# Kernel optimization log

Hardware: AMD Instinct MI355X
Metric: run time of the kernel (lower is better)

Reference implementation:

```python
import jax, jax.numpy as jnp
import numpy as np
from jax import lax

KS = 11          # kernel_size
SIGMA = 1.5
MAX_VAL = 1.0
C1 = (0.01 * MAX_VAL) ** 2
C2 = (0.03 * MAX_VAL) ** 2
EPS = 1e-12
PAD = KS // 2    # use_padding=True -> reflect pad


def _gaussian_kernel3d():
    ax = jnp.arange(KS, dtype=jnp.float32) - (KS - 1) / 2.0
    g = jnp.exp(-(ax[:, None, None] ** 2 + ax[None, :, None] ** 2 + ax[None, None, :] ** 2)
                / (2.0 * SIGMA ** 2))
    return g / g.sum()  # (KS, KS, KS)


def setup_inputs() -> dict:
    key = jax.random.key(0)
    k1, k2 = jax.random.split(key)
    shape = (2, 1, 160, 160, 160)
    source = jax.random.uniform(k1, shape, dtype=jnp.float32)
    reference_vol = jax.random.uniform(k2, shape, dtype=jnp.float32)
    return {"source": source, "reference": reference_vol}


def reference(source, reference):
    B, C, H, W, D = source.shape
    # reflect pad spatial dims (torch 'reflect' == numpy 'reflect')
    pad_cfg = ((0, 0), (0, 0), (PAD, PAD), (PAD, PAD), (PAD, PAD))
    src = jnp.pad(source, pad_cfg, mode="reflect")
    ref = jnp.pad(reference, pad_cfg, mode="reflect")

    # fuse the 5 depthwise convolutions into one grouped conv over stacked channels
    stacked = jnp.concatenate([src, ref, src * src, ref * ref, src * ref], axis=1)  # (B,5C,...)
    kern = _gaussian_kernel3d()[None, None]                      # (1,1,KS,KS,KS)
    kern = jnp.tile(kern, (5 * C, 1, 1, 1, 1))                   # (5C,1,KS,KS,KS)
    out = lax.conv_general_dilated(
        stacked, kern, window_strides=(1, 1, 1), padding="VALID",
        feature_group_count=5 * C,
        dimension_numbers=("NCDHW", "OIDHW", "NCDHW"))           # (B,5C,H,W,D)

    mu1 = out[:, 0 * C:1 * C]
    mu2 = out[:, 1 * C:2 * C]
    m11 = out[:, 2 * C:3 * C]
    m22 = out[:, 3 * C:4 * C]
    m12 = out[:, 4 * C:5 * C]

    mu1_sq = mu1 * mu1
    mu2_sq = mu2 * mu2
    mu1_mu2 = mu1 * mu2
    sigma1_sq = m11 - mu1_sq
    sigma2_sq = m22 - mu2_sq
    sigma12 = m12 - mu1_mu2

    numerator = (2.0 * mu1_mu2 + C1) * (2.0 * sigma12 + C2)
    denominator = (mu1_sq + mu2_sq + C1) * (sigma1_sq + sigma2_sq + C2)
    ssim = numerator / (denominator + EPS)
    return 1.0 - ssim.mean()
```

## Files before the change

kernel.cpp:

```cpp
#include <hip/hip_runtime.h>
#include <math.h>

#define HH 160
#define WW 160
#define DD 160
#define VOL (HH*WW*DD)
#define KS 11
#define PAD 5
#define NBATCH 2
#define NTOT (NBATCH*VOL)

#define WT 16
#define DT 16
#define HT 32
#define WPN (WT + 2*PAD)
#define NSTEP (HT + 2*PAD)
#define RS 68
#define P01S 36
#define P4S 16
#define RAW_W (WPN*RS)
#define P01_W (WPN*P01S)
#define P4_W  (WPN*P4S)

typedef float v2f __attribute__((ext_vector_type(2)));
typedef float v4f __attribute__((ext_vector_type(4)));

struct Wts { float w[KS]; };

__device__ __forceinline__ int mirror(int i, int n) {
    if (i < 0) i = -i;
    if (i >= n) i = 2*n - 2 - i;
    return i;
}

__device__ __forceinline__ v2f pk_fma(v2f a, v2f b, v2f c) {
    v2f d; asm("v_pk_fma_f32 %0, %1, %2, %3" : "=v"(d) : "v"(a), "v"(b), "v"(c)); return d;
}
__device__ __forceinline__ v2f pk_mul(v2f a, v2f b) {
    v2f d; asm("v_pk_mul_f32 %0, %1, %2" : "=v"(d) : "v"(a), "v"(b)); return d;
}
__device__ __forceinline__ v2f pk_add(v2f a, v2f b) {
    v2f d; asm("v_pk_add_f32 %0, %1, %2" : "=v"(d) : "v"(a), "v"(b)); return d;
}

__global__ void init_out(float* out) {
    if (threadIdx.x == 0 && blockIdx.x == 0) out[0] = 1.0f;
}

__global__ __launch_bounds__(256) void fused(const float* __restrict__ src,
                                             const float* __restrict__ ref,
                                             float* __restrict__ out,
                                             Wts wts, float scale) {
    __shared__ float raw [2*RAW_W];
    __shared__ float pl01[2*P01_W];
    __shared__ float pl23[2*P01_W];
    __shared__ float pl4 [2*P4_W];

    const int bx  = blockIdx.x;
    const int dt_ = bx % (DD/DT);
    const int wt_ = (bx / (DD/DT)) % (WW/WT);
    const int ht_ = (bx / ((DD/DT)*(WW/WT))) % (HH/HT);
    const int b   = bx / ((DD/DT)*(WW/WT)*(HH/HT));
    const int d0 = dt_*DT, w0 = wt_*WT, h0 = ht_*HT;

    const int  dbase = (d0 == 0) ? 0 : ((d0 == DD-DT) ? DD-32 : d0-8);
    const bool dedge = (d0 == 0) || (d0 == DD-DT);

    const int tid = threadIdx.x;
    const float* __restrict__ sp = src + (size_t)b*VOL;
    const float* __restrict__ rp = ref + (size_t)b*VOL;

    const bool sact = (tid < WPN*8);
    const int  swp = tid >> 3, sq = tid & 7;
    const int  sgoff  = mirror(w0 - PAD + (sact ? swp : 0), WW)*DD + dbase + sq*4;
    const int  srawof = swp*RS + sq*8;

    const int  p_dl  = tid & 15;
    const int  p_wp0 = tid >> 4;
    const bool p_act1 = (tid < WPN*DT - 256);
    const int  pw0_01 = p_wp0*P01S + 2*p_dl;
    const int  pw0_4  = p_wp0*P4S  + p_dl;
    const int  pw1_01 = (p_wp0+16)*P01S + 2*p_dl;
    const int  pw1_4  = (p_wp0+16)*P4S  + p_dl;

    int eoff[KS];
    if (dedge) {
#pragma unroll
        for (int k = 0; k < KS; ++k)
            eoff[k] = 2*(mirror(d0 + p_dl - PAD + k, DD) - dbase);
    }

    const int wl = tid >> 4, dl2 = tid & 15;

    v2f wpk[KS];
#pragma unroll
    for (int k = 0; k < KS; ++k) { wpk[k].x = wts.w[k]; wpk[k].y = wts.w[k]; }

    v2f acc01[KS], acc23[KS];
    float acc4[KS];
#pragma unroll
    for (int s = 0; s < KS; ++s) {
        acc01[s] = (v2f)0.f; acc23[s] = (v2f)0.f; acc4[s] = 0.f;
    }

    v4f ra = (v4f)0.f, rb_ = (v4f)0.f;
    if (sact) {
        const size_t o0 = (size_t)mirror(h0 - PAD, HH)*(WW*DD) + sgoff;
        ra  = *reinterpret_cast<const v4f*>(sp + o0);
        rb_ = *reinterpret_cast<const v4f*>(rp + o0);
        v4f c0, c1;
        c0.x=ra.x; c0.y=rb_.x; c0.z=ra.y; c0.w=rb_.y;
        c1.x=ra.z; c1.y=rb_.z; c1.z=ra.w; c1.w=rb_.w;
        *reinterpret_cast<v4f*>(&raw[srawof])     = c0;
        *reinterpret_cast<v4f*>(&raw[srawof + 4]) = c1;
        const size_t o1 = (size_t)mirror(h0 - PAD + 1, HH)*(WW*DD) + sgoff;
        ra  = *reinterpret_cast<const v4f*>(sp + o1);
        rb_ = *reinterpret_cast<const v4f*>(rp + o1);
    }
    __syncthreads();

    float ssum = 0.f;
    int rawRd = 0, rawWr = RAW_W, po01 = 0, po4 = 0;

    for (int tb = 0; tb < 44; tb += 11) {
#pragma unroll
        for (int ts = 0; ts < 11; ++ts) {
            const int t = tb + ts;
            if (t < NSTEP) {
                if (sact) {
                    v4f c0, c1;
                    c0.x=ra.x; c0.y=rb_.x; c0.z=ra.y; c0.w=rb_.y;
                    c1.x=ra.z; c1.y=rb_.z; c1.z=ra.w; c1.w=rb_.w;
                    *reinterpret_cast<v4f*>(&raw[rawWr + srawof])     = c0;
                    *reinterpret_cast<v4f*>(&raw[rawWr + srawof + 4]) = c1;
                    const size_t on = (size_t)mirror(h0 - PAD + t + 2, HH)*(WW*DD) + sgoff;
                    ra  = *reinterpret_cast<const v4f*>(sp + on);
                    rb_ = *reinterpret_cast<const v4f*>(rp + on);
                }

                v2f mu_a=(v2f)0.f, mm_a=(v2f)0.f, mu_b=(v2f)0.f, mm_b=(v2f)0.f;
                float m12a=0.f, m12b=0.f;
                if (!dedge) {
                    const float* r0 = &raw[rawRd + p_wp0*RS + 2*p_dl + 6];
                    const float* r1 = r0 + 16*RS;
#pragma unroll
                    for (int k = 0; k < KS; ++k) {
                        v2f sr = *reinterpret_cast<const v2f*>(r0 + 2*k);
                        v2f p  = pk_mul(sr, wpk[k]);
                        mu_a = pk_add(mu_a, p);
                        mm_a = pk_fma(p, sr, mm_a);
                        m12a = fmaf(p.x, sr.y, m12a);
                    }
                    if (p_act1) {
#pragma unroll
                        for (int k = 0; k < KS; ++k) {
                            v2f sr = *reinterpret_cast<const v2f*>(r1 + 2*k);
                            v2f p  = pk_mul(sr, wpk[k]);
                            mu_b = pk_add(mu_b, p);
                            mm_b = pk_fma(p, sr, mm_b);
                            m12b = fmaf(p.x, sr.y, m12b);
                        }
                    }
                } else {
                    const float* rb0 = &raw[rawRd + p_wp0*RS];
                    const float* rb1 = rb0 + 16*RS;
#pragma unroll
                    for (int k = 0; k < KS; ++k) {
                        v2f sr = *reinterpret_cast<const v2f*>(rb0 + eoff[k]);
                        v2f p  = pk_mul(sr, wpk[k]);
                        mu_a = pk_add(mu_a, p);
                        mm_a = pk_fma(p, sr, mm_a);
                        m12a = fmaf(p.x, sr.y, m12a);
                        if (p_act1) {
                            v2f sr2 = *reinterpret_cast<const v2f*>(rb1 + eoff[k]);
                            v2f p2  = pk_mul(sr2, wpk[k]);
                            mu_b = pk_add(mu_b, p2);
                            mm_b = pk_fma(p2, sr2, mm_b);
                            m12b = fmaf(p2.x, sr2.y, m12b);
                        }
                    }
                }
                *reinterpret_cast<v2f*>(&pl01[po01 + pw0_01]) = mu_a;
                *reinterpret_cast<v2f*>(&pl23[po01 + pw0_01]) = mm_a;
                pl4[po4 + pw0_4] = m12a;
                if (p_act1) {
                    *reinterpret_cast<v2f*>(&pl01[po01 + pw1_01]) = mu_b;
                    *reinterpret_cast<v2f*>(&pl23[po01 + pw1_01]) = mm_b;
                    pl4[po4 + pw1_4] = m12b;
                }

                __syncthreads();

                {
                    v2f v01 = (v2f)0.f, v23 = (v2f)0.f;
                    float v4v = 0.f;
                    const float* q01 = &pl01[po01 + wl*P01S + 2*dl2];
                    const float* q23 = &pl23[po01 + wl*P01S + 2*dl2];
                    const float* q4  = &pl4 [po4  + wl*P4S  + dl2];
#pragma unroll
                    for (int k = 0; k < KS; ++k) {
                        v2f w = wpk[k];
                        v01 = pk_fma(*reinterpret_cast<const v2f*>(q01 + k*P01S), w, v01);
                        v23 = pk_fma(*reinterpret_cast<const v2f*>(q23 + k*P01S), w, v23);
                        v4v = fmaf(w.x, q4[k*P4S], v4v);
                    }
#pragma unroll
                    for (int m = 0; m < 11; ++m) {
                        const int slot = (ts + m) % 11;
                        v2f wt = wpk[10 - m];
                        acc01[slot] = pk_fma(v01, wt, acc01[slot]);
                        acc23[slot] = pk_fma(v23, wt, acc23[slot]);
                        acc4[slot]  = fmaf(wt.x, v4v, acc4[slot]);
                    }
                    if (t >= 10) {
                        float mu1 = acc01[ts].x, mu2 = acc01[ts].y;
                        float m11 = acc23[ts].x, m22 = acc23[ts].y, m12 = acc4[ts];
                        float mu1sq = mu1*mu1, mu2sq = mu2*mu2, mu12 = mu1*mu2;
                        float s1 = m11 - mu1sq, s2 = m22 - mu2sq, s12 = m12 - mu12;
                        const float C1 = 1e-4f, C2 = 9e-4f;
                        float num = (2.f*mu12 + C1) * (2.f*s12 + C2);
                        float den = (mu1sq + mu2sq + C1) * (s1 + s2 + C2) + 1e-12f;
                        float inv = __builtin_amdgcn_rcpf(den);
                        inv = inv * (2.0f - den * inv);
                        ssum = fmaf(num, inv, ssum);
                    }
                    acc01[ts] = (v2f)0.f; acc23[ts] = (v2f)0.f; acc4[ts] = 0.f;
                }

                rawRd ^= RAW_W; rawWr ^= RAW_W; po01 ^= P01_W; po4 ^= P4_W;
            }
        }
    }

#pragma unroll
    for (int off = 32; off > 0; off >>= 1)
        ssum += __shfl_down(ssum, off, 64);
    __shared__ float lsum[4];
    int lane = tid & 63, wid = tid >> 6;
    if (lane == 0) lsum[wid] = ssum;
    __syncthreads();
    if (tid == 0)
        atomicAdd(out, -(lsum[0]+lsum[1]+lsum[2]+lsum[3]) * scale);
}

extern "C" void kernel_launch(void* const* d_in, const int* in_sizes, int n_in,
                              void* d_out, int out_size, void* d_ws, size_t ws_size,
                              hipStream_t stream) {
    const float* src = (const float*)d_in[0];
    const float* ref = (const float*)d_in[1];
    float* out = (float*)d_out;

    Wts wts;
    {
        double g[KS], s = 0.0;
        for (int i = 0; i < KS; ++i) {
            double a = (double)i - (KS - 1) / 2.0;
            g[i] = exp(-(a * a) / (2.0 * 1.5 * 1.5));
            s += g[i];
        }
        for (int i = 0; i < KS; ++i) wts.w[i] = (float)(g[i] / s);
    }

    const float scale = 1.0f / (float)NTOT;

    init_out<<<1, 64, 0, stream>>>(out);
    const int g = NBATCH * (HH/HT) * (WW/WT) * (DD/DT);
    fused<<<g, 256, 0, stream>>>(src, ref, out, wts, scale);
}
```

Before: 212.5 us.

## Compute two adjacent depth outputs per thread in first conv pass

The depth-direction convolution pass now gives each of the 208 active threads two adjacent depth outputs (8 threads per W row). Each thread reads 12 shared-memory values and reuses them for both outputs, where before a thread did one output and some threads made a second pass over a separate row. The change also switches the packed FMA/add inline asm to in-place accumulator constraints, adds a launch_bounds occupancy hint of 4 blocks, and aligns the shared arrays. The aim is fewer LDS reads and better thread balance, at the cost of more registers per thread and a possible bank-conflict shift from the wider stores.

```diff
diff --git a/kernel.cpp b/kernel.cpp
--- a/kernel.cpp
+++ b/kernel.cpp
@@ -33,28 +33,28 @@
     return i;
 }
 
-__device__ __forceinline__ v2f pk_fma(v2f a, v2f b, v2f c) {
-    v2f d; asm("v_pk_fma_f32 %0, %1, %2, %3" : "=v"(d) : "v"(a), "v"(b), "v"(c)); return d;
+__device__ __forceinline__ void pk_fma_acc(v2f& c, v2f a, v2f b) {
+    asm("v_pk_fma_f32 %0, %1, %2, %0" : "+v"(c) : "v"(a), "v"(b));
+}
+__device__ __forceinline__ void pk_add_acc(v2f& c, v2f a) {
+    asm("v_pk_add_f32 %0, %0, %1" : "+v"(c) : "v"(a));
 }
 __device__ __forceinline__ v2f pk_mul(v2f a, v2f b) {
     v2f d; asm("v_pk_mul_f32 %0, %1, %2" : "=v"(d) : "v"(a), "v"(b)); return d;
 }
-__device__ __forceinline__ v2f pk_add(v2f a, v2f b) {
-    v2f d; asm("v_pk_add_f32 %0, %1, %2" : "=v"(d) : "v"(a), "v"(b)); return d;
-}
 
 __global__ void init_out(float* out) {
     if (threadIdx.x == 0 && blockIdx.x == 0) out[0] = 1.0f;
 }
 
-__global__ __launch_bounds__(256) void fused(const float* __restrict__ src,
-                                             const float* __restrict__ ref,
-                                             float* __restrict__ out,
-                                             Wts wts, float scale) {
-    __shared__ float raw [2*RAW_W];
-    __shared__ float pl01[2*P01_W];
-    __shared__ float pl23[2*P01_W];
-    __shared__ float pl4 [2*P4_W];
+__global__ __launch_bounds__(256, 4) void fused(const float* __restrict__ src,
+                                                const float* __restrict__ ref,
+                                                float* __restrict__ out,
+                                                Wts wts, float scale) {
+    __shared__ __align__(16) float raw [2*RAW_W];
+    __shared__ __align__(16) float pl01[2*P01_W];
+    __shared__ __align__(16) float pl23[2*P01_W];
+    __shared__ __align__(16) float pl4 [2*P4_W];
 
     const int bx  = blockIdx.x;
     const int dt_ = bx % (DD/DT);
@@ -75,19 +75,17 @@
     const int  sgoff  = mirror(w0 - PAD + (sact ? swp : 0), WW)*DD + dbase + sq*4;
     const int  srawof = swp*RS + sq*8;
 
-    const int  p_dl  = tid & 15;
-    const int  p_wp0 = tid >> 4;
-    const bool p_act1 = (tid < WPN*DT - 256);
-    const int  pw0_01 = p_wp0*P01S + 2*p_dl;
-    const int  pw0_4  = p_wp0*P4S  + p_dl;
-    const int  pw1_01 = (p_wp0+16)*P01S + 2*p_dl;
-    const int  pw1_4  = (p_wp0+16)*P4S  + p_dl;
-
-    int eoff[KS];
+    const int  p_wp  = tid >> 3;
+    const int  p_dlp = tid & 7;
+    const int  pA01  = p_wp*P01S + 4*p_dlp;
+    const int  pA4   = p_wp*P4S  + 2*p_dlp;
+    const int  p_rbase = p_wp*RS + 6 + 4*p_dlp;
+
+    int eoff[12];
     if (dedge) {
 #pragma unroll
-        for (int k = 0; k < KS; ++k)
-            eoff[k] = 2*(mirror(d0 + p_dl - PAD + k, DD) - dbase);
+        for (int j = 0; j < 12; ++j)
+            eoff[j] = 2*(mirror(d0 + 2*p_dlp - PAD + j, DD) - dbase);
     }
 
     const int wl = tid >> 4, dl2 = tid & 15;
@@ -136,57 +134,52 @@
                     const size_t on = (size_t)mirror(h0 - PAD + t + 2, HH)*(WW*DD) + sgoff;
                     ra  = *reinterpret_cast<const v4f*>(sp + on);
                     rb_ = *reinterpret_cast<const v4f*>(rp + on);
-                }
-
-                v2f mu_a=(v2f)0.f, mm_a=(v2f)0.f, mu_b=(v2f)0.f, mm_b=(v2f)0.f;
-                float m12a=0.f, m12b=0.f;
-                if (!dedge) {
-                    const float* r0 = &raw[rawRd + p_wp0*RS + 2*p_dl + 6];
-                    const float* r1 = r0 + 16*RS;
-#pragma unroll
-                    for (int k = 0; k < KS; ++k) {
-                        v2f sr = *reinterpret_cast<const v2f*>(r0 + 2*k);
-                        v2f p  = pk_mul(sr, wpk[k]);
-                        mu_a = pk_add(mu_a, p);
-                        mm_a = pk_fma(p, sr, mm_a);
-                        m12a = fmaf(p.x, sr.y, m12a);
-                    }
-                    if (p_act1) {
-#pragma unroll
-                        for (int k = 0; k < KS; ++k) {
-                            v2f sr = *reinterpret_cast<const v2f*>(r1 + 2*k);
-                            v2f p  = pk_mul(sr, wpk[k]);
-                            mu_b = pk_add(mu_b, p);
-                            mm_b = pk_fma(p, sr, mm_b);
-                            m12b = fmaf(p.x, sr.y, m12b);
+
+                    v2f muA=(v2f)0.f, mmA=(v2f)0.f, muB=(v2f)0.f, mmB=(v2f)0.f;
+                    float m12A=0.f, m12B=0.f;
+                    if (!dedge) {
+                        const float* r0 = &raw[rawRd + p_rbase];
+#pragma unroll
+                        for (int j = 0; j < 12; ++j) {
+                            v2f sr = *reinterpret_cast<const v2f*>(r0 + 2*j);
+                            if (j < 11) {
+                                v2f p = pk_mul(sr, wpk[j]);
+                                pk_add_acc(muA, p);
+                                pk_fma_acc(mmA, p, sr);
+                                m12A = fmaf(p.x, sr.y, m12A);
+                            }
+                            if (j > 0) {
+                                v2f p = pk_mul(sr, wpk[j-1]);
+                                pk_add_acc(muB, p);
+                                pk_fma_acc(mmB, p, sr);
+                                m12B = fmaf(p.x, sr.y, m12B);
+                            }
                         }
-                    }
-                } else {
-                    const float* rb0 = &raw[rawRd + p_wp0*RS];
-                    const float* rb1 = rb0 + 16*RS;
-#pragma unroll
-                    for (int k = 0; k < KS; ++k) {
-                        v2f sr = *reinterpret_cast<const v2f*>(rb0 + eoff[k]);
-                        v2f p  = pk_mul(sr, wpk[k]);
-                        mu_a = pk_add(mu_a, p);
-                        mm_a = pk_fma(p, sr, mm_a);
-                        m12a = fmaf(p.x, sr.y, m12a);
-                        if (p_act1) {
-                            v2f sr2 = *reinterpret_cast<const v2f*>(rb1 + eoff[k]);
-                            v2f p2  = pk_mul(sr2, wpk[k]);
-                            mu_b = pk_add(mu_b, p2);
-                            mm_b = pk_fma(p2, sr2, mm_b);
-                            m12b = fmaf(p2.x, sr2.y, m12b);
+                    } else {
+                        const float* r0 = &raw[rawRd + p_wp*RS];
+#pragma unroll
+                        for (int j = 0; j < 12; ++j) {
+                            v2f sr = *reinterpret_cast<const v2f*>(r0 + eoff[j]);
+                            if (j < 11) {
+                                v2f p = pk_mul(sr, wpk[j]);
+                                pk_add_acc(muA, p);
+                                pk_fma_acc(mmA, p, sr);
+                                m12A = fmaf(p.x, sr.y, m12A);
+                            }
+                            if (j > 0) {
+                                v2f p = pk_mul(sr, wpk[j-1]);
+                                pk_add_acc(muB, p);
+                                pk_fma_acc(mmB, p, sr);
+                                m12B = fmaf(p.x, sr.y, m12B);
+                            }
                         }
                     }
-                }
-                *reinterpret_cast<v2f*>(&pl01[po01 + pw0_01]) = mu_a;
-                *reinterpret_cast<v2f*>(&pl23[po01 + pw0_01]) = mm_a;
-                pl4[po4 + pw0_4] = m12a;
-                if (p_act1) {
-                    *reinterpret_cast<v2f*>(&pl01[po01 + pw1_01]) = mu_b;
-                    *reinterpret_cast<v2f*>(&pl23[po01 + pw1_01]) = mm_b;
-                    pl4[po4 + pw1_4] = m12b;
+                    *reinterpret_cast<v2f*>(&pl01[po01 + pA01])     = muA;
+                    *reinterpret_cast<v2f*>(&pl01[po01 + pA01 + 2]) = muB;
+                    *reinterpret_cast<v2f*>(&pl23[po01 + pA01])     = mmA;
+                    *reinterpret_cast<v2f*>(&pl23[po01 + pA01 + 2]) = mmB;
+                    v2f m12w; m12w.x = m12A; m12w.y = m12B;
+                    *reinterpret_cast<v2f*>(&pl4[po4 + pA4])        = m12w;
                 }
 
                 __syncthreads();
@@ -200,16 +193,16 @@
 #pragma unroll
                     for (int k = 0; k < KS; ++k) {
                         v2f w = wpk[k];
-                        v01 = pk_fma(*reinterpret_cast<const v2f*>(q01 + k*P01S), w, v01);
-                        v23 = pk_fma(*reinterpret_cast<const v2f*>(q23 + k*P01S), w, v23);
+                        pk_fma_acc(v01, *reinterpret_cast<const v2f*>(q01 + k*P01S), w);
+                        pk_fma_acc(v23, *reinterpret_cast<const v2f*>(q23 + k*P01S), w);
                         v4v = fmaf(w.x, q4[k*P4S], v4v);
                     }
 #pragma unroll
                     for (int m = 0; m < 11; ++m) {
                         const int slot = (ts + m) % 11;
                         v2f wt = wpk[10 - m];
-                        acc01[slot] = pk_fma(v01, wt, acc01[slot]);
-                        acc23[slot] = pk_fma(v23, wt, acc23[slot]);
+                        pk_fma_acc(acc01[slot], v01, wt);
+                        pk_fma_acc(acc23[slot], v23, wt);
                         acc4[slot]  = fmaf(wt.x, v4v, acc4[slot]);
                     }
                     if (t >= 10) {
```

New measurement: 385.0 us. +81.2%, slower.
